# Performance work log

Hardware: AMD Instinct MI355X
Metric: run time of the kernel (lower is better)

## Reference

```python
import jax, jax.numpy as jnp
import numpy as np

N_WIN = 8
NUM_HEADS = 8
TOPK = 4
D_MODEL = 128
SCALE = D_MODEL ** (-0.5)


def setup_inputs() -> dict:
    key = jax.random.key(0)
    k1, k2 = jax.random.split(key)
    cv_feature = jax.random.normal(k1, (1, 128, 128, 128), dtype=jnp.float32)
    mv_feature = jax.random.normal(k2, (1, 2, 128, 128, 128), dtype=jnp.float32)
    return {"cv_feature": cv_feature, "mv_feature": mv_feature}


def reference(cv_feature, mv_feature):
    # cv_feature: [N, H, W, C] query view; mv_feature: [N, V, H, W, C] multi-view KV
    N, H, W, C = cv_feature.shape
    V = mv_feature.shape[1]
    j = i = N_WIN
    h, w = H // j, W // i
    p2, w2 = j * i, h * w
    ch = C // NUM_HEADS  # per-head dim

    # window partition: n (j h) (i w) c -> n (j i) h w c
    cv_patch = cv_feature.reshape(N, j, h, i, w, C).transpose(0, 1, 3, 2, 4, 5).reshape(N, p2, h, w, C)
    mv_patch = mv_feature.reshape(N, V, j, h, i, w, C).transpose(0, 1, 2, 4, 3, 5, 6).reshape(N, V, p2, h, w, C)

    q_pix = cv_patch.reshape(N, p2, w2, C)          # [N, p2, w2, C]
    kv_pix = mv_patch.reshape(N, V, p2, w2, C)      # [N, V, p2, w2, C]

    # window-level descriptors (means) -> routing logits
    q_win = cv_patch.mean(axis=(2, 3))              # [N, p2, C]
    k_win = mv_patch.mean(axis=(3, 4))              # [N, V, p2, C]

    # TopK routing (detached in original; forward math identical)
    k_flat = k_win.reshape(N, V * p2, C)
    attn_logit = jnp.einsum('npc,nqc->npq', q_win * SCALE, k_flat)  # [N, p2, V*p2]
    topk_logit, r_idx = jax.lax.top_k(attn_logit, TOPK)
    r_weight = jax.nn.softmax(topk_logit, axis=-1)  # computed by module, unused downstream

    # KV gather of selected windows: [N, p2, topk, w2, C]
    kv_flat = kv_pix.reshape(N, V * p2, w2, C)
    kv_sel = kv_flat[jnp.arange(N)[:, None, None], r_idx]

    # per-window multi-head attention over topk*w2 gathered tokens
    q = q_pix.reshape(N, p2, w2, NUM_HEADS, ch)
    kv = kv_sel.reshape(N, p2, TOPK * w2, NUM_HEADS, ch)
    attn = jnp.einsum('npwmc,npxmc->npmwx', q * SCALE, kv)  # [N, p2, m, w2, topk*w2]
    attn = jax.nn.softmax(attn, axis=-1)
    out = jnp.einsum('npmwx,npxmc->npwmc', attn, kv)        # [N, p2, w2, m, ch]

    # merge windows back: n (j i) (h w) c -> n (j h) (i w) c
    out = out.reshape(N, j, i, h, w, C).transpose(0, 1, 3, 2, 4, 5).reshape(N, H, W, C)
    return out
```

## Files before the change

kernel.cpp:

```cpp
#include <hip/hip_runtime.h>

#define HH_ 128
#define WW_ 128
#define CC_ 128
#define P2 64
#define W2 256
#define NH 8
#define CH 16
#define NV 2
#define TOPK 4
#define SCALE 0.08838834764831845f

typedef unsigned short u16;
typedef unsigned int   u32;
typedef _Float16 h4 __attribute__((ext_vector_type(4)));
typedef float    f4 __attribute__((ext_vector_type(4)));

__device__ float g_means[(P2 + NV * P2) * CC_];
__device__ int2  g_part[64];
__device__ int   g_mode;
__device__ int   g_amb;

__device__ inline u16 f2b(float v) {
    union { float f; u32 u; } x; x.f = v;
    u32 r = x.u + 0x7FFFu + ((x.u >> 16) & 1u);
    return (u16)(r >> 16);
}
__device__ inline float b2f(u16 h) {
    union { u32 u; float f; } x; x.u = (u32)h << 16; return x.f;
}
__device__ inline float h2f(u16 h) {
    u32 s = (h >> 15) & 1u, e = (h >> 10) & 31u, m = h & 1023u;
    float v;
    if (e == 0)       v = m * 5.9604644775e-8f;
    else if (e == 31) v = 65504.f;
    else { union { u32 u; float f; } x; x.u = ((e + 112u) << 23) | (m << 13); v = x.f; }
    return s ? -v : v;
}
__device__ inline u16 f2h(float v) {
    union { float f; u32 u; } x; x.f = v;
    u32 s = (x.u >> 16) & 0x8000u;
    int  e = (int)((x.u >> 23) & 0xFF) - 112;
    u32  m = x.u & 0x7FFFFF;
    if (e >= 31) return (u16)(s | 0x7BFF);
    if (e <= 0) {
        if (e < -10) return (u16)s;
        m |= 0x800000u;
        int sh = 14 - e;
        u32 r = m >> sh, rem = m & ((1u << sh) - 1u), half = 1u << (sh - 1);
        if (rem > half || (rem == half && (r & 1))) r++;
        return (u16)(s | r);
    }
    u32 r = ((u32)e << 10) | (m >> 13), rem = m & 0x1FFFu;
    if (rem > 0x1000u || (rem == 0x1000u && (r & 1))) r++;
    return (u16)(s | r);
}

__device__ inline void load16(const void* __restrict__ src, size_t off, int mode,
                              float* __restrict__ f) {
    if (mode == 0) {
        const float4* p4 = (const float4*)((const float*)src + off);
#pragma unroll
        for (int i = 0; i < 4; ++i) {
            float4 v = p4[i];
            f[4 * i] = v.x; f[4 * i + 1] = v.y; f[4 * i + 2] = v.z; f[4 * i + 3] = v.w;
        }
    } else {
        const uint4* p4 = (const uint4*)((const u16*)src + off);
#pragma unroll
        for (int i = 0; i < 2; ++i) {
            uint4 v = p4[i];
            u32 wd[4] = { v.x, v.y, v.z, v.w };
#pragma unroll
            for (int j = 0; j < 4; ++j) {
                u16 lo = (u16)(wd[j] & 0xFFFFu), hi = (u16)(wd[j] >> 16);
                f[8 * i + 2 * j]     = (mode == 1) ? b2f(lo) : h2f(lo);
                f[8 * i + 2 * j + 1] = (mode == 1) ? b2f(hi) : h2f(hi);
            }
        }
    }
}

__device__ inline void load4(const void* __restrict__ src, size_t off, int mode,
                             float* __restrict__ f) {
    if (mode == 0) {
        float4 v = *(const float4*)((const float*)src + off);
        f[0] = v.x; f[1] = v.y; f[2] = v.z; f[3] = v.w;
    } else {
        uint2 v = *(const uint2*)((const u16*)src + off);
        u32 w0 = v.x, w1 = v.y;
        if (mode == 1) {
            f[0] = b2f((u16)w0); f[1] = b2f((u16)(w0 >> 16));
            f[2] = b2f((u16)w1); f[3] = b2f((u16)(w1 >> 16));
        } else {
            f[0] = h2f((u16)w0); f[1] = h2f((u16)(w0 >> 16));
            f[2] = h2f((u16)w1); f[3] = h2f((u16)(w1 >> 16));
        }
    }
}

__device__ inline void store4(void* __restrict__ out, size_t off, int mode,
                              const float* __restrict__ r) {
    if (mode == 0) {
        *(float4*)((float*)out + off) = make_float4(r[0], r[1], r[2], r[3]);
    } else {
        u32 w0, w1;
        if (mode == 1) {
            w0 = (u32)f2b(r[0]) | ((u32)f2b(r[1]) << 16);
            w1 = (u32)f2b(r[2]) | ((u32)f2b(r[3]) << 16);
        } else {
            w0 = (u32)f2h(r[0]) | ((u32)f2h(r[1]) << 16);
            w1 = (u32)f2h(r[2]) | ((u32)f2h(r[3]) << 16);
        }
        *(uint2*)((u16*)out + off) = make_uint2(w0, w1);
    }
}

__global__ void detect_sample(const void* __restrict__ cv, int n) {
    __shared__ int bc[2];
    int tid = threadIdx.x, k = blockIdx.x;
    if (tid < 2) bc[tid] = 0;
    __syncthreads();
    int lim32 = n / 2;
    int lim16 = n / 2;
    u32 r = ((u32)(tid + k * 257) * 2654435761u);
    int j32 = (int)(r % (u32)lim32);
    float a = fabsf(((const float*)cv)[j32]);
    bool c0 = (a >= 1e-4f && a <= 1e4f);
    int j16 = 2 * (int)((r >> 8) % (u32)lim16);
    float b = fabsf(b2f(((const u16*)cv)[j16]));
    bool c1 = (b >= 1e-4f && b <= 1e4f);
    unsigned long long b0 = __ballot(c0);
    unsigned long long b1 = __ballot(c1);
    if ((tid & 63) == 0) {
        atomicAdd(&bc[0], __popcll(b0));
        atomicAdd(&bc[1], __popcll(b1));
    }
    __syncthreads();
    if (tid == 0) g_part[k] = make_int2(bc[0], bc[1]);
}

__global__ void detect_final() {
    int tid = threadIdx.x;
    int2 v = g_part[tid];
    int c0 = v.x, c1 = v.y;
#pragma unroll
    for (int off = 32; off >= 1; off >>= 1) {
        c0 += __shfl_down(c0, off);
        c1 += __shfl_down(c1, off);
    }
    if (tid == 0) {
        const float T = 256.f * 64.f;
        float f0 = c0 / T, f1 = c1 / T;
        int mode, amb = 0;
        if (f1 >= 0.85f) mode = 1;
        else if (f0 >= 0.80f) mode = 0;
        else mode = 2;
        if ((f1 > 0.60f && f1 < 0.85f) || (mode != 1 && f0 > 0.65f && f0 < 0.80f)) amb = 1;
        g_mode = mode; g_amb = amb;
    }
}

__global__ __launch_bounds__(512) void win_mean_kernel(const void* __restrict__ cv,
                                                       const void* __restrict__ mv) {
    __shared__ float sred[512];
    int mode = g_mode;
    int row = blockIdx.x;
    int tid = threadIdx.x;
    int c = tid & 127, q4 = tid >> 7;
    const void* src; size_t voff = 0; int p;
    if (row < P2) { p = row; src = cv; }
    else { int r = row - P2; voff = (size_t)(r >> 6) * HH_ * WW_ * CC_; p = r & 63; src = mv; }
    int jj = p >> 3, ii = p & 7;
    size_t base = voff + ((size_t)(jj * 16 + q4 * 4) * WW_ + ii * 16) * CC_ + c;
    float acc = 0.f;
    if (mode == 0) {
        const float* sp = (const float*)src;
        for (int hh = 0; hh < 4; ++hh) {
#pragma unroll
            for (int ww = 0; ww < 16; ++ww)
                acc += sp[base + ((size_t)hh * WW_ + ww) * CC_];
        }
    } else if (mode == 1) {
        const u16* sp = (const u16*)src;
        for (int hh = 0; hh < 4; ++hh) {
#pragma unroll
            for (int ww = 0; ww < 16; ++ww)
                acc += b2f(sp[base + ((size_t)hh * WW_ + ww) * CC_]);
        }
    } else {
        const u16* sp = (const u16*)src;
        for (int hh = 0; hh < 4; ++hh) {
#pragma unroll
            for (int ww = 0; ww < 16; ++ww)
                acc += h2f(sp[base + ((size_t)hh * WW_ + ww) * CC_]);
        }
    }
    sred[tid] = acc;
    __syncthreads();
    if (tid < 128) {
        float s = sred[tid] + sred[tid + 128] + sred[tid + 256] + sred[tid + 384];
        g_means[row * CC_ + tid] = s * (1.0f / 256.0f);
    }
}

__global__ __launch_bounds__(512, 4) void attn_kernel(const void* __restrict__ cv,
                                                      const void* __restrict__ mv,
                                                      void* __restrict__ out) {
#define VSTR 1028
    __shared__ _Float16 vt[32][VSTR];
    __shared__ float slog[NV * P2];
    __shared__ int   sridx[TOPK];

    int mode = g_mode;
    int p = blockIdx.x >> 3, m = blockIdx.x & 7;
    int tid = threadIdx.x;

    {
        int t  = tid >> 2;
        int cs = (tid & 3) << 5;
        const float4* qw = (const float4*)(g_means + p * CC_ + cs);
        const float4* kw = (const float4*)(g_means + (P2 + t) * CC_ + cs);
        float a = 0.f;
#pragma unroll
        for (int i = 0; i < 8; ++i) {
            float4 qv = qw[i], kv4 = kw[i];
            a += qv.x * kv4.x + qv.y * kv4.y + qv.z * kv4.z + qv.w * kv4.w;
        }
        a += __shfl_down(a, 2, 4);
        a += __shfl_down(a, 1, 4);
        if ((tid & 3) == 0) slog[t] = a;
    }
    __syncthreads();
    if (tid == 0) {
#pragma unroll
        for (int k = 0; k < TOPK; ++k) {
            int best = 0; float bv = slog[0];
            for (int q2 = 1; q2 < NV * P2; ++q2)
                if (slog[q2] > bv) { bv = slog[q2]; best = q2; }
            sridx[k] = best;
            slog[best] = -3.0e38f;
        }
    }
    __syncthreads();

    int rwin[TOPK];
#pragma unroll
    for (int k = 0; k < TOPK; ++k) rwin[k] = sridx[k] & 127;

    int jj = p >> 3, ii = p & 7;

#pragma unroll
    for (int it = 0; it < 2; ++it) {
        int kr = tid + it * 512;
        int g  = kr >> 8, t2 = kr & 255;
        int t  = rwin[g];
        int v  = t >> 6, pp = t & 63;
        int jj2 = pp >> 3, ii2 = pp & 7;
        int hh = t2 >> 4, ww = t2 & 15;
        size_t kvbase = (((size_t)v * HH_ + jj2 * 16 + hh) * WW_ + (ii2 * 16 + ww)) * CC_ + m * CH;
        float f[CH];
        load16(mv, kvbase, mode, f);
#pragma unroll
        for (int c = 0; c < CH; ++c) {
            _Float16 hi = (_Float16)f[c];
            _Float16 lo = (_Float16)(f[c] - (float)hi);
            vt[c][kr]      = hi;
            vt[c + 16][kr] = lo;
        }
    }

    int wv = tid >> 6, l = tid & 63;
    int lg = l >> 4, lr = l & 15;
    h4 qhi[2], qlo[2];
#pragma unroll
    for (int qi = 0; qi < 2; ++qi) {
        int qrow = wv * 32 + qi * 16 + lr;
        int hh = qrow >> 4, ww = qrow & 15;
        size_t pix = (size_t)(jj * 16 + hh) * WW_ + (ii * 16 + ww);
        float qf[4];
        load4(cv, pix * CC_ + m * CH + 4 * lg, mode, qf);
#pragma unroll
        for (int i = 0; i < 4; ++i) {
            float x = qf[i] * SCALE;
            _Float16 hi = (_Float16)x;
            qhi[qi][i] = hi;
            qlo[qi][i] = (_Float16)(x - (float)hi);
        }
    }
    __syncthreads();

    f4 Oacc0 = {0.f, 0.f, 0.f, 0.f};
    f4 Oacc1 = {0.f, 0.f, 0.f, 0.f};
    float lp0 = 0.f, lp1 = 0.f;

#pragma unroll 2
    for (int kt = 0; kt < 64; ++kt) {
        int g = kt >> 4;
        int t = rwin[g];
        int v = t >> 6, pp = t & 63;
        int jj2 = pp >> 3, ii2 = pp & 7;
        int hh2 = kt & 15;
        size_t kvbase = (((size_t)v * HH_ + jj2 * 16 + hh2) * WW_ + (ii2 * 16 + lr)) * CC_
                        + m * CH + 4 * lg;
        float kf[4];
        load4(mv, kvbase, mode, kf);
        h4 khi, klo;
#pragma unroll
        for (int i = 0; i < 4; ++i) {
            _Float16 hi = (_Float16)kf[i];
            khi[i] = hi;
            klo[i] = (_Float16)(kf[i] - (float)hi);
        }

        int key0 = kt * 16;
        h4 vhi = *(const h4*)&vt[lr][key0 + 4 * lg];
        h4 vlo = *(const h4*)&vt[lr + 16][key0 + 4 * lg];

        {
            f4 sc = {0.f, 0.f, 0.f, 0.f};
            sc = __builtin_amdgcn_mfma_f32_16x16x16f16(khi, qhi[0], sc, 0, 0, 0);
            sc = __builtin_amdgcn_mfma_f32_16x16x16f16(khi, qlo[0], sc, 0, 0, 0);
            sc = __builtin_amdgcn_mfma_f32_16x16x16f16(klo, qhi[0], sc, 0, 0, 0);
            h4 phi, plo;
#pragma unroll
            for (int r = 0; r < 4; ++r) {
                float s  = fminf(sc[r], 11.0f);
                float pe = __expf(s);
                lp0 += pe;
                _Float16 ph = (_Float16)pe;
                phi[r] = ph;
                plo[r] = (_Float16)(pe - (float)ph);
            }
            Oacc0 = __builtin_amdgcn_mfma_f32_16x16x16f16(vhi, phi, Oacc0, 0, 0, 0);
            Oacc0 = __builtin_amdgcn_mfma_f32_16x16x16f16(vhi, plo, Oacc0, 0, 0, 0);
            Oacc0 = __builtin_amdgcn_mfma_f32_16x16x16f16(vlo, phi, Oacc0, 0, 0, 0);
        }
        {
            f4 sc = {0.f, 0.f, 0.f, 0.f};
            sc = __builtin_amdgcn_mfma_f32_16x16x16f16(khi, qhi[1], sc, 0, 0, 0);
            sc = __builtin_amdgcn_mfma_f32_16x16x16f16(khi, qlo[1], sc, 0, 0, 0);
            sc = __builtin_amdgcn_mfma_f32_16x16x16f16(klo, qhi[1], sc, 0, 0, 0);
            h4 phi, plo;
#pragma unroll
            for (int r = 0; r < 4; ++r) {
                float s  = fminf(sc[r], 11.0f);
                float pe = __expf(s);
                lp1 += pe;
                _Float16 ph = (_Float16)pe;
                phi[r] = ph;
                plo[r] = (_Float16)(pe - (float)ph);
            }
            Oacc1 = __builtin_amdgcn_mfma_f32_16x16x16f16(vhi, phi, Oacc1, 0, 0, 0);
            Oacc1 = __builtin_amdgcn_mfma_f32_16x16x16f16(vhi, plo, Oacc1, 0, 0, 0);
            Oacc1 = __builtin_amdgcn_mfma_f32_16x16x16f16(vlo, phi, Oacc1, 0, 0, 0);
        }
    }

#pragma unroll
    for (int qi = 0; qi < 2; ++qi) {
        float lt = (qi == 0) ? lp0 : lp1;
        lt += __shfl_xor(lt, 16);
        lt += __shfl_xor(lt, 32);
        float inv = 1.0f / fmaxf(lt, 1e-30f);
        f4 Oa = (qi == 0) ? Oacc0 : Oacc1;
        float res[4];
#pragma unroll
        for (int r = 0; r < 4; ++r)
            res[r] = fminf(fmaxf(Oa[r] * inv, -1000.f), 1000.f);
        int qrow = wv * 32 + qi * 16 + lr;
        int hh = qrow >> 4, ww = qrow & 15;
        size_t pix = (size_t)(jj * 16 + hh) * WW_ + (ii * 16 + ww);
        store4(out, pix * CC_ + m * CH + 4 * lg, mode, res);
    }
#undef VSTR
}

extern "C" void kernel_launch(void* const* d_in, const int* in_sizes, int n_in,
                              void* d_out, int out_size, void* d_ws, size_t ws_size,
                              hipStream_t stream) {
    const void* cv = d_in[0];
    const void* mv = d_in[1];
    int n_cv = in_sizes[0];
    if (n_in >= 2 && in_sizes[0] > in_sizes[1]) { cv = d_in[1]; mv = d_in[0]; n_cv = in_sizes[1]; }
    (void)d_ws; (void)ws_size; (void)out_size;

    detect_sample<<<64, 256, 0, stream>>>(cv, n_cv);
    detect_final<<<1, 64, 0, stream>>>();
    win_mean_kernel<<<192, 512, 0, stream>>>(cv, mv);
    attn_kernel<<<P2 * NH, 512, 0, stream>>>(cv, mv, d_out);
}
```

Before: 155.0 us.

## Switch split-precision attention MFMAs to bf16 16x16x32 with K prefetch

Replaces the three-MFMA fp16 hi/lo split products with two bf16 16x16x32 MFMAs that pack the hi and lo parts into one 8-wide operand with swapped halves. V is stored in shared memory in a fragment-ready layout, and K loads are prefetched two iterations ahead in registers. The data-type mode is made a template parameter so each specialized body has no runtime mode branches. Matrix instruction count per tile drops, at the cost of bf16 truncation error in place of fp16 rounding and a wider exp clamp.

```diff
diff --git a/kernel.cpp b/kernel.cpp
--- a/kernel.cpp
+++ b/kernel.cpp
@@ -13,8 +13,10 @@
 
 typedef unsigned short u16;
 typedef unsigned int   u32;
-typedef _Float16 h4 __attribute__((ext_vector_type(4)));
-typedef float    f4 __attribute__((ext_vector_type(4)));
+typedef short s8v __attribute__((ext_vector_type(8)));
+typedef float f4  __attribute__((ext_vector_type(4)));
+
+union FRAG { uint4 q; u32 u[4]; s8v v; };
 
 __device__ float g_means[(P2 + NV * P2) * CC_];
 __device__ int2  g_part[64];
@@ -56,9 +58,32 @@
     return (u16)(s | r);
 }
 
-__device__ inline void load16(const void* __restrict__ src, size_t off, int mode,
-                              float* __restrict__ f) {
-    if (mode == 0) {
+__device__ inline u32 pkhi(float a, float b) {
+    union { float f; u32 u; } xa, xb; xa.f = a; xb.f = b;
+    return (xa.u >> 16) | (xb.u & 0xFFFF0000u);
+}
+__device__ inline float hipart(float a) {
+    union { float f; u32 u; } x; x.f = a; x.u &= 0xFFFF0000u; return x.f;
+}
+
+template<int MODE>
+__device__ inline float4 loadf4(const void* __restrict__ src, int off) {
+    if (MODE == 0) return *(const float4*)((const float*)src + off);
+    uint2 v = *(const uint2*)((const u16*)src + off);
+    float4 r;
+    if (MODE == 1) {
+        r.x = b2f((u16)v.x); r.y = b2f((u16)(v.x >> 16));
+        r.z = b2f((u16)v.y); r.w = b2f((u16)(v.y >> 16));
+    } else {
+        r.x = h2f((u16)v.x); r.y = h2f((u16)(v.x >> 16));
+        r.z = h2f((u16)v.y); r.w = h2f((u16)(v.y >> 16));
+    }
+    return r;
+}
+
+template<int MODE>
+__device__ inline void load16t(const void* __restrict__ src, int off, float* __restrict__ f) {
+    if (MODE == 0) {
         const float4* p4 = (const float4*)((const float*)src + off);
 #pragma unroll
         for (int i = 0; i < 4; ++i) {
@@ -74,44 +99,24 @@
 #pragma unroll
             for (int j = 0; j < 4; ++j) {
                 u16 lo = (u16)(wd[j] & 0xFFFFu), hi = (u16)(wd[j] >> 16);
-                f[8 * i + 2 * j]     = (mode == 1) ? b2f(lo) : h2f(lo);
-                f[8 * i + 2 * j + 1] = (mode == 1) ? b2f(hi) : h2f(hi);
+                f[8 * i + 2 * j]     = (MODE == 1) ? b2f(lo) : h2f(lo);
+                f[8 * i + 2 * j + 1] = (MODE == 1) ? b2f(hi) : h2f(hi);
             }
         }
     }
 }
 
-__device__ inline void load4(const void* __restrict__ src, size_t off, int mode,
-                             float* __restrict__ f) {
-    if (mode == 0) {
-        float4 v = *(const float4*)((const float*)src + off);
-        f[0] = v.x; f[1] = v.y; f[2] = v.z; f[3] = v.w;
+template<int MODE>
+__device__ inline void store4t(void* __restrict__ out, int off, const float* __restrict__ r) {
+    if (MODE == 0) {
+        *(float4*)((float*)out + off) = make_float4(r[0], r[1], r[2], r[3]);
+    } else if (MODE == 1) {
+        u32 w0 = (u32)f2b(r[0]) | ((u32)f2b(r[1]) << 16);
+        u32 w1 = (u32)f2b(r[2]) | ((u32)f2b(r[3]) << 16);
+        *(uint2*)((u16*)out + off) = make_uint2(w0, w1);
     } else {
-        uint2 v = *(const uint2*)((const u16*)src + off);
-        u32 w0 = v.x, w1 = v.y;
-        if (mode == 1) {
-            f[0] = b2f((u16)w0); f[1] = b2f((u16)(w0 >> 16));
-            f[2] = b2f((u16)w1); f[3] = b2f((u16)(w1 >> 16));
-        } else {
-            f[0] = h2f((u16)w0); f[1] = h2f((u16)(w0 >> 16));
-            f[2] = h2f((u16)w1); f[3] = h2f((u16)(w1 >> 16));
-        }
-    }
-}
-
-__device__ inline void store4(void* __restrict__ out, size_t off, int mode,
-                              const float* __restrict__ r) {
-    if (mode == 0) {
-        *(float4*)((float*)out + off) = make_float4(r[0], r[1], r[2], r[3]);
-    } else {
-        u32 w0, w1;
-        if (mode == 1) {
-            w0 = (u32)f2b(r[0]) | ((u32)f2b(r[1]) << 16);
-            w1 = (u32)f2b(r[2]) | ((u32)f2b(r[3]) << 16);
-        } else {
-            w0 = (u32)f2h(r[0]) | ((u32)f2h(r[1]) << 16);
-            w1 = (u32)f2h(r[2]) | ((u32)f2h(r[3]) << 16);
-        }
+        u32 w0 = (u32)f2h(r[0]) | ((u32)f2h(r[1]) << 16);
+        u32 w1 = (u32)f2h(r[2]) | ((u32)f2h(r[3]) << 16);
         *(uint2*)((u16*)out + off) = make_uint2(w0, w1);
     }
 }
@@ -204,156 +209,122 @@
     }
 }
 
-__global__ __launch_bounds__(512, 4) void attn_kernel(const void* __restrict__ cv,
-                                                      const void* __restrict__ mv,
-                                                      void* __restrict__ out) {
-#define VSTR 1028
-    __shared__ _Float16 vt[32][VSTR];
-    __shared__ float slog[NV * P2];
-    __shared__ int   sridx[TOPK];
-
-    int mode = g_mode;
-    int p = blockIdx.x >> 3, m = blockIdx.x & 7;
-    int tid = threadIdx.x;
-
-    {
-        int t  = tid >> 2;
-        int cs = (tid & 3) << 5;
-        const float4* qw = (const float4*)(g_means + p * CC_ + cs);
-        const float4* kw = (const float4*)(g_means + (P2 + t) * CC_ + cs);
-        float a = 0.f;
-#pragma unroll
-        for (int i = 0; i < 8; ++i) {
-            float4 qv = qw[i], kv4 = kw[i];
-            a += qv.x * kv4.x + qv.y * kv4.y + qv.z * kv4.z + qv.w * kv4.w;
-        }
-        a += __shfl_down(a, 2, 4);
-        a += __shfl_down(a, 1, 4);
-        if ((tid & 3) == 0) slog[t] = a;
-    }
-    __syncthreads();
-    if (tid == 0) {
-#pragma unroll
-        for (int k = 0; k < TOPK; ++k) {
-            int best = 0; float bv = slog[0];
-            for (int q2 = 1; q2 < NV * P2; ++q2)
-                if (slog[q2] > bv) { bv = slog[q2]; best = q2; }
-            sridx[k] = best;
-            slog[best] = -3.0e38f;
-        }
-    }
-    __syncthreads();
-
-    int rwin[TOPK];
-#pragma unroll
-    for (int k = 0; k < TOPK; ++k) rwin[k] = sridx[k] & 127;
-
+template<int MODE>
+__device__ void attn_body(const void* __restrict__ cv, const void* __restrict__ mv,
+                          void* __restrict__ out, int p, int m, int tid,
+                          u32 (* __restrict__ vfrag)[64][4], const int* __restrict__ rwin) {
     int jj = p >> 3, ii = p & 7;
 
 #pragma unroll
     for (int it = 0; it < 2; ++it) {
         int kr = tid + it * 512;
-        int g  = kr >> 8, t2 = kr & 255;
-        int t  = rwin[g];
-        int v  = t >> 6, pp = t & 63;
+        int kt = kr >> 4, r = kr & 15, g = r >> 2, iofs = r & 3;
+        int t = rwin[kr >> 8];
+        int v = t >> 6, pp = t & 63;
         int jj2 = pp >> 3, ii2 = pp & 7;
-        int hh = t2 >> 4, ww = t2 & 15;
-        size_t kvbase = (((size_t)v * HH_ + jj2 * 16 + hh) * WW_ + (ii2 * 16 + ww)) * CC_ + m * CH;
+        int hh = (kr >> 4) & 15, ww = r;
+        int kvbase = ((v * HH_ + jj2 * 16 + hh) * WW_ + ii2 * 16 + ww) * CC_ + m * CH;
         float f[CH];
-        load16(mv, kvbase, mode, f);
+        load16t<MODE>(mv, kvbase, f);
 #pragma unroll
         for (int c = 0; c < CH; ++c) {
-            _Float16 hi = (_Float16)f[c];
-            _Float16 lo = (_Float16)(f[c] - (float)hi);
-            vt[c][kr]      = hi;
-            vt[c + 16][kr] = lo;
+            union { float ff; u32 uu; } x; x.ff = f[c];
+            u16 hi = (u16)(x.uu >> 16);
+            union { float ff; u32 uu; } y; y.ff = f[c] - hipart(f[c]);
+            u16 lo = (u16)(y.uu >> 16);
+            u16* s = (u16*)&vfrag[kt][g * 16 + c][0];
+            s[iofs] = hi; s[4 + iofs] = lo;
         }
     }
 
     int wv = tid >> 6, l = tid & 63;
     int lg = l >> 4, lr = l & 15;
-    h4 qhi[2], qlo[2];
+    FRAG qf1[2], qf2[2];
 #pragma unroll
     for (int qi = 0; qi < 2; ++qi) {
         int qrow = wv * 32 + qi * 16 + lr;
         int hh = qrow >> 4, ww = qrow & 15;
-        size_t pix = (size_t)(jj * 16 + hh) * WW_ + (ii * 16 + ww);
-        float qf[4];
-        load4(cv, pix * CC_ + m * CH + 4 * lg, mode, qf);
-#pragma unroll
-        for (int i = 0; i < 4; ++i) {
-            float x = qf[i] * SCALE;
-            _Float16 hi = (_Float16)x;
-            qhi[qi][i] = hi;
-            qlo[qi][i] = (_Float16)(x - (float)hi);
-        }
-    }
-    __syncthreads();
-
+        int pix = (jj * 16 + hh) * WW_ + (ii * 16 + ww);
+        float4 qv = loadf4<MODE>(cv, pix * CC_ + m * CH + 4 * lg);
+        float q0 = qv.x * SCALE, q1 = qv.y * SCALE, q2 = qv.z * SCALE, q3 = qv.w * SCALE;
+        u32 h01 = pkhi(q0, q1), h23 = pkhi(q2, q3);
+        u32 l01 = pkhi(q0 - hipart(q0), q1 - hipart(q1));
+        u32 l23 = pkhi(q2 - hipart(q2), q3 - hipart(q3));
+        qf1[qi].u[0] = h01; qf1[qi].u[1] = h23; qf1[qi].u[2] = l01; qf1[qi].u[3] = l23;
+        qf2[qi].u[0] = l01; qf2[qi].u[1] = l23; qf2[qi].u[2] = h01; qf2[qi].u[3] = h23;
+    }
+
+    int wb0, wb1, wb2, wb3;
+#define MKWB(G, W) { int t = rwin[G]; int v = t >> 6, pp = t & 63;            \
+        int jj2 = pp >> 3, ii2 = pp & 7;                                      \
+        W = ((v * HH_ + jj2 * 16) * WW_ + ii2 * 16 + lr) * CC_ + m * CH + 4 * lg; }
+    MKWB(0, wb0) MKWB(1, wb1) MKWB(2, wb2) MKWB(3, wb3)
+#undef MKWB
+
+    __syncthreads();
+
+    float4 kA0 = loadf4<MODE>(mv, wb0);
+    float4 kA1 = loadf4<MODE>(mv, wb0 + WW_ * CC_);
     f4 Oacc0 = {0.f, 0.f, 0.f, 0.f};
     f4 Oacc1 = {0.f, 0.f, 0.f, 0.f};
     float lp0 = 0.f, lp1 = 0.f;
+    const u32* vbase = &vfrag[0][l][0];
 
 #pragma unroll 2
     for (int kt = 0; kt < 64; ++kt) {
-        int g = kt >> 4;
-        int t = rwin[g];
-        int v = t >> 6, pp = t & 63;
-        int jj2 = pp >> 3, ii2 = pp & 7;
-        int hh2 = kt & 15;
-        size_t kvbase = (((size_t)v * HH_ + jj2 * 16 + hh2) * WW_ + (ii2 * 16 + lr)) * CC_
-                        + m * CH + 4 * lg;
-        float kf[4];
-        load4(mv, kvbase, mode, kf);
-        h4 khi, klo;
-#pragma unroll
-        for (int i = 0; i < 4; ++i) {
-            _Float16 hi = (_Float16)kf[i];
-            khi[i] = hi;
-            klo[i] = (_Float16)(kf[i] - (float)hi);
-        }
-
-        int key0 = kt * 16;
-        h4 vhi = *(const h4*)&vt[lr][key0 + 4 * lg];
-        h4 vlo = *(const h4*)&vt[lr + 16][key0 + 4 * lg];
+        float4 kc = (kt & 1) ? kA1 : kA0;
+        {
+            int ktn = kt + 2; ktn = (ktn > 63) ? 63 : ktn;
+            int a = (ktn < 16) ? wb0 : (ktn < 32) ? wb1 : (ktn < 48) ? wb2 : wb3;
+            a += (ktn & 15) * (WW_ * CC_);
+            float4 nv = loadf4<MODE>(mv, a);
+            if (kt & 1) kA1 = nv; else kA0 = nv;
+        }
+        FRAG kf;
+        kf.u[0] = pkhi(kc.x, kc.y);
+        kf.u[1] = pkhi(kc.z, kc.w);
+        kf.u[2] = pkhi(kc.x - hipart(kc.x), kc.y - hipart(kc.y));
+        kf.u[3] = pkhi(kc.z - hipart(kc.z), kc.w - hipart(kc.w));
+        FRAG vf;
+        vf.q = *(const uint4*)(vbase + kt * 256);
 
         {
             f4 sc = {0.f, 0.f, 0.f, 0.f};
-            sc = __builtin_amdgcn_mfma_f32_16x16x16f16(khi, qhi[0], sc, 0, 0, 0);
-            sc = __builtin_amdgcn_mfma_f32_16x16x16f16(khi, qlo[0], sc, 0, 0, 0);
-            sc = __builtin_amdgcn_mfma_f32_16x16x16f16(klo, qhi[0], sc, 0, 0, 0);
-            h4 phi, plo;
-#pragma unroll
-            for (int r = 0; r < 4; ++r) {
-                float s  = fminf(sc[r], 11.0f);
-                float pe = __expf(s);
-                lp0 += pe;
-                _Float16 ph = (_Float16)pe;
-                phi[r] = ph;
-                plo[r] = (_Float16)(pe - (float)ph);
-            }
-            Oacc0 = __builtin_amdgcn_mfma_f32_16x16x16f16(vhi, phi, Oacc0, 0, 0, 0);
-            Oacc0 = __builtin_amdgcn_mfma_f32_16x16x16f16(vhi, plo, Oacc0, 0, 0, 0);
-            Oacc0 = __builtin_amdgcn_mfma_f32_16x16x16f16(vlo, phi, Oacc0, 0, 0, 0);
+            sc = __builtin_amdgcn_mfma_f32_16x16x32_bf16(kf.v, qf1[0].v, sc, 0, 0, 0);
+            sc = __builtin_amdgcn_mfma_f32_16x16x32_bf16(kf.v, qf2[0].v, sc, 0, 0, 0);
+            float pe0 = __expf(fminf(sc[0], 20.f));
+            float pe1 = __expf(fminf(sc[1], 20.f));
+            float pe2 = __expf(fminf(sc[2], 20.f));
+            float pe3 = __expf(fminf(sc[3], 20.f));
+            lp0 += (pe0 + pe1) + (pe2 + pe3);
+            FRAG pf1, pf2;
+            pf1.u[0] = pkhi(pe0, pe1);
+            pf1.u[1] = pkhi(pe2, pe3);
+            pf1.u[2] = pkhi(pe0 - hipart(pe0), pe1 - hipart(pe1));
+            pf1.u[3] = pkhi(pe2 - hipart(pe2), pe3 - hipart(pe3));
+            pf2.u[0] = pf1.u[2]; pf2.u[1] = pf1.u[3];
+            pf2.u[2] = pf1.u[0]; pf2.u[3] = pf1.u[1];
+            Oacc0 = __builtin_amdgcn_mfma_f32_16x16x32_bf16(vf.v, pf1.v, Oacc0, 0, 0, 0);
+            Oacc0 = __builtin_amdgcn_mfma_f32_16x16x32_bf16(vf.v, pf2.v, Oacc0, 0, 0, 0);
         }
         {
             f4 sc = {0.f, 0.f, 0.f, 0.f};
-            sc = __builtin_amdgcn_mfma_f32_16x16x16f16(khi, qhi[1], sc, 0, 0, 0);
-            sc = __builtin_amdgcn_mfma_f32_16x16x16f16(khi, qlo[1], sc, 0, 0, 0);
-            sc = __builtin_amdgcn_mfma_f32_16x16x16f16(klo, qhi[1], sc, 0, 0, 0);
-            h4 phi, plo;
-#pragma unroll
-            for (int r = 0; r < 4; ++r) {
-                float s  = fminf(sc[r], 11.0f);
-                float pe = __expf(s);
-                lp1 += pe;
-                _Float16 ph = (_Float16)pe;
-                phi[r] = ph;
-                plo[r] = (_Float16)(pe - (float)ph);
-            }
-            Oacc1 = __builtin_amdgcn_mfma_f32_16x16x16f16(vhi, phi, Oacc1, 0, 0, 0);
-            Oacc1 = __builtin_amdgcn_mfma_f32_16x16x16f16(vhi, plo, Oacc1, 0, 0, 0);
-            Oacc1 = __builtin_amdgcn_mfma_f32_16x16x16f16(vlo, phi, Oacc1, 0, 0, 0);
+            sc = __builtin_amdgcn_mfma_f32_16x16x32_bf16(kf.v, qf1[1].v, sc, 0, 0, 0);
+            sc = __builtin_amdgcn_mfma_f32_16x16x32_bf16(kf.v, qf2[1].v, sc, 0, 0, 0);
+            float pe0 = __expf(fminf(sc[0], 20.f));
+            float pe1 = __expf(fminf(sc[1], 20.f));
+            float pe2 = __expf(fminf(sc[2], 20.f));
+            float pe3 = __expf(fminf(sc[3], 20.f));
+            lp1 += (pe0 + pe1) + (pe2 + pe3);
+            FRAG pf1, pf2;
+            pf1.u[0] = pkhi(pe0, pe1);
+            pf1.u[1] = pkhi(pe2, pe3);
+            pf1.u[2] = pkhi(pe0 - hipart(pe0), pe1 - hipart(pe1));
+            pf1.u[3] = pkhi(pe2 - hipart(pe2), pe3 - hipart(pe3));
+            pf2.u[0] = pf1.u[2]; pf2.u[1] = pf1.u[3];
+            pf2.u[2] = pf1.u[0]; pf2.u[3] = pf1.u[1];
+            Oacc1 = __builtin_amdgcn_mfma_f32_16x16x32_bf16(vf.v, pf1.v, Oacc1, 0, 0, 0);
+            Oacc1 = __builtin_amdgcn_mfma_f32_16x16x32_bf16(vf.v, pf2.v, Oacc1, 0, 0, 0);
         }
     }
 
@@ -370,10 +341,57 @@
             res[r] = fminf(fmaxf(Oa[r] * inv, -1000.f), 1000.f);
         int qrow = wv * 32 + qi * 16 + lr;
         int hh = qrow >> 4, ww = qrow & 15;
-        size_t pix = (size_t)(jj * 16 + hh) * WW_ + (ii * 16 + ww);
-        store4(out, pix * CC_ + m * CH + 4 * lg, mode, res);
-    }
-#undef VSTR
+        int pix = (jj * 16 + hh) * WW_ + (ii * 16 + ww);
+        store4t<MODE>(out, pix * CC_ + m * CH + 4 * lg, res);
+    }
+}
+
+__global__ __launch_bounds__(512, 4) void attn_kernel(const void* __restrict__ cv,
+                                                      const void* __restrict__ mv,
+                                                      void* __restrict__ out) {
+    __shared__ u32 vfrag[64][64][4];
+    __shared__ float slog[NV * P2];
+    __shared__ int   sridx[TOPK];
+
+    int mode = g_mode;
+    int p = blockIdx.x >> 3, m = blockIdx.x & 7;
+    int tid = threadIdx.x;
+
+    {
+        int t  = tid >> 2;
+        int cs = (tid & 3) << 5;
+        const float4* qw = (const float4*)(g_means + p * CC_ + cs);
+        const float4* kw = (const float4*)(g_means + (P2 + t) * CC_ + cs);
+        float a = 0.f;
+#pragma unroll
+        for (int i = 0; i < 8; ++i) {
+            float4 qv = qw[i], kv4 = kw[i];
+            a += qv.x * kv4.x + qv.y * kv4.y + qv.z * kv4.z + qv.w * kv4.w;
+        }
+        a += __shfl_down(a, 2, 4);
+        a += __shfl_down(a, 1, 4);
+        if ((tid & 3) == 0) slog[t] = a;
+    }
+    __syncthreads();
+    if (tid == 0) {
+#pragma unroll
+        for (int k = 0; k < TOPK; ++k) {
+            int best = 0; float bv = slog[0];
+            for (int q2 = 1; q2 < NV * P2; ++q2)
+                if (slog[q2] > bv) { bv = slog[q2]; best = q2; }
+            sridx[k] = best;
+            slog[best] = -3.0e38f;
+        }
+    }
+    __syncthreads();
+
+    int rwin[TOPK];
+#pragma unroll
+    for (int k = 0; k < TOPK; ++k) rwin[k] = sridx[k] & 127;
+
+    if (mode == 0)      attn_body<0>(cv, mv, out, p, m, tid, vfrag, rwin);
+    else if (mode == 1) attn_body<1>(cv, mv, out, p, m, tid, vfrag, rwin);
+    else                attn_body<2>(cv, mv, out, p, m, tid, vfrag, rwin);
 }
 
 extern "C" void kernel_launch(void* const* d_in, const int* in_sizes, int n_in,
```

New measurement: 150.5 us. -2.9%, faster.
